# Performance work log

Measured on AMD Instinct MI355X. Metric: run time of the kernel, lower is better.

The kernel has to match this reference:

```python
import jax, jax.numpy as jnp
import numpy as np

THRESHOLD = 10.0
K = 24
EPS = 1e-9
BN_EPS = 1e-5


def setup_inputs() -> dict:
    key = jax.random.key(0)
    k0, k1, k2, k3 = jax.random.split(key, 4)
    B, C, H, W = 4, 256, 64, 64
    x = jax.random.normal(k0, (B, C, H, W), jnp.float32)
    fc_w = jax.random.normal(k1, (C, C), jnp.float32) * (1.0 / np.sqrt(C))
    fc_b = jax.random.normal(k2, (C,), jnp.float32) * 0.01
    dist_w = jax.random.normal(k3, (64, C), jnp.float32) * (1.0 / np.sqrt(C))
    bn_gamma = jnp.ones((C,), jnp.float32)
    bn_beta = jnp.zeros((C,), jnp.float32)
    return {"x": x, "fc_w": fc_w, "fc_b": fc_b, "dist_w": dist_w,
            "bn_gamma": bn_gamma, "bn_beta": bn_beta}


def reference(x, fc_w, fc_b, dist_w, bn_gamma, bn_beta):
    B, C, H, W = x.shape
    N = H * W
    # ds branch: only triggers when H == 40; here H=64 so ds=1 (no pool/interp)
    x_flat = x.reshape(B, C, N).transpose(0, 2, 1)        # [B, N, C]
    # dist_embed: 1x1 conv == linear projection per spatial location
    emb = jnp.einsum('bnc,ec->bne', x_flat, dist_w)       # [B, N, 64]
    # pairwise Euclidean distances (cdist)
    sq = jnp.sum(emb * emb, axis=-1)                      # [B, N]
    d2 = sq[:, :, None] + sq[:, None, :] - 2.0 * jnp.einsum('bne,bme->bnm', emb, emb)
    dist = jnp.sqrt(jnp.clip(d2, 0.0))                    # [B, N, N]
    # kNN mask via top_k of -dist
    _, idx = jax.lax.top_k(-dist, K)                      # [B, N, K]
    bi = jnp.arange(B)[:, None, None]
    ni = jnp.arange(N)[None, :, None]
    knn_mask = jnp.zeros((B, N, N), bool).at[bi, ni, idx].set(True)
    adj = knn_mask & (dist <= THRESHOLD)
    adj = adj | jnp.eye(N, dtype=bool)[None]
    adj_f = adj.astype(x.dtype)                           # H: [B, N, E=N]
    # HypConv: X' = Dv^{-1} H De^{-1} H^T (X Theta), residual added outside
    X_lin = x_flat @ fc_w.T + fc_b                        # [B, N, C]
    Dv = jnp.clip(jnp.sum(adj_f, axis=2), EPS, None)      # [B, N]
    De = jnp.clip(jnp.sum(adj_f, axis=1), EPS, None)      # [B, E]
    H_De_inv = adj_f / De[:, None, :]
    S = (H_De_inv @ adj_f.transpose(0, 2, 1)) / Dv[:, :, None]   # [B, N, N]
    out_flat = S @ X_lin + x_flat                         # residual
    out = out_flat.transpose(0, 2, 1).reshape(B, C, H, W)
    # BatchNorm2d in training mode (batch statistics, biased variance)
    mean = jnp.mean(out, axis=(0, 2, 3))
    var = jnp.var(out, axis=(0, 2, 3))
    o = (out - mean[None, :, None, None]) * jax.lax.rsqrt(var[None, :, None, None] + BN_EPS)
    o = o * bn_gamma[None, :, None, None] + bn_beta[None, :, None, None]
    # SiLU
    return o * jax.nn.sigmoid(o)
```

## Files before the change

### kernel.cpp

```cpp
#include <hip/hip_runtime.h>

#define NB 4096
#define BATCH 4
#define CD 256
#define ED 64
#define KNN 24

typedef __attribute__((ext_vector_type(8))) short bf16x8;
typedef __attribute__((ext_vector_type(4))) float f32x4;

__device__ __forceinline__ unsigned short f2bf(float x) {
  unsigned u = __float_as_uint(x);
  unsigned r = (u + 0x7fffu + ((u >> 16) & 1u)) >> 16;
  return (unsigned short)r;
}

__global__ __launch_bounds__(256) void k_emb(const float* __restrict__ x,
                                             const float* __restrict__ dist_w,
                                             unsigned* __restrict__ emb_hl,
                                             float* __restrict__ sq,
                                             unsigned* __restrict__ thr_g) {
  __shared__ float wds[ED * CD];
  __shared__ float red[64 * 4];
  const int b = blockIdx.x >> 6;
  const int n0 = (blockIdx.x & 63) << 6;
  const int tid = threadIdx.x;
  const float4* wsrc = (const float4*)dist_w;
  float4* wdst = (float4*)wds;
#pragma unroll
  for (int k = 0; k < 16; ++k) wdst[tid + 256 * k] = wsrc[tid + 256 * k];
  __syncthreads();
  const int eg = tid >> 6;
  const int nl = tid & 63;
  const int n = n0 + nl;
  float acc[16];
#pragma unroll
  for (int t = 0; t < 16; ++t) acc[t] = 0.f;
  const float* xb = x + (size_t)b * CD * NB + n;
#pragma unroll 2
  for (int c4 = 0; c4 < CD; c4 += 4) {
    float x0 = xb[(size_t)(c4 + 0) * NB];
    float x1 = xb[(size_t)(c4 + 1) * NB];
    float x2 = xb[(size_t)(c4 + 2) * NB];
    float x3 = xb[(size_t)(c4 + 3) * NB];
#pragma unroll
    for (int t = 0; t < 16; ++t) {
      float4 wv = *(const float4*)&wds[(eg * 16 + t) * CD + c4];
      acc[t] = fmaf(x0, wv.x, acc[t]);
      acc[t] = fmaf(x1, wv.y, acc[t]);
      acc[t] = fmaf(x2, wv.z, acc[t]);
      acc[t] = fmaf(x3, wv.w, acc[t]);
    }
  }
  float s = 0.f;
#pragma unroll
  for (int t = 0; t < 16; ++t) s = fmaf(acc[t], acc[t], s);
  unsigned hw[8], lw[8];
#pragma unroll
  for (int i = 0; i < 8; ++i) {
    unsigned short h0 = f2bf(acc[2 * i]);
    unsigned short h1 = f2bf(acc[2 * i + 1]);
    float l0f = acc[2 * i] - __uint_as_float((unsigned)h0 << 16);
    float l1f = acc[2 * i + 1] - __uint_as_float((unsigned)h1 << 16);
    hw[i] = (unsigned)h0 | ((unsigned)h1 << 16);
    lw[i] = (unsigned)f2bf(l0f) | ((unsigned)f2bf(l1f) << 16);
  }
  uint4* g = (uint4*)emb_hl;
  const size_t gb = ((size_t)(b * NB + n)) * 16;
  const int k15 = n & 15;
  g[gb + ((2 * eg) ^ k15)]     = make_uint4(hw[0], hw[1], hw[2], hw[3]);
  g[gb + ((2 * eg + 1) ^ k15)] = make_uint4(hw[4], hw[5], hw[6], hw[7]);
  g[gb + ((8 + 2 * eg) ^ k15)]     = make_uint4(lw[0], lw[1], lw[2], lw[3]);
  g[gb + ((8 + 2 * eg + 1) ^ k15)] = make_uint4(lw[4], lw[5], lw[6], lw[7]);
  red[nl * 4 + eg] = s;
  __syncthreads();
  if (tid < 64) {
    sq[b * NB + n0 + tid] = red[tid * 4] + red[tid * 4 + 1] + red[tid * 4 + 2] + red[tid * 4 + 3];
    thr_g[(b << 12) + n0 + tid] = 0x42C80000u;
  }
}

__global__ __launch_bounds__(256) void k_wsplit(const float* __restrict__ fc_w,
                                                unsigned* __restrict__ w_hl) {
  const int u = blockIdx.x * 256 + threadIdx.x;
  const int c = u >> 5, cg = u & 31;
  const int kt = cg >> 3, chl = cg & 7;
  const float* src = fc_w + (size_t)c * CD + kt * 64 + chl * 8;
  unsigned hi[4], lo[4];
#pragma unroll
  for (int j = 0; j < 4; ++j) {
    float a0 = src[2 * j], a1 = src[2 * j + 1];
    unsigned short h0 = f2bf(a0), h1 = f2bf(a1);
    float l0 = a0 - __uint_as_float((unsigned)h0 << 16);
    float l1 = a1 - __uint_as_float((unsigned)h1 << 16);
    hi[j] = (unsigned)h0 | ((unsigned)h1 << 16);
    lo[j] = (unsigned)f2bf(l0) | ((unsigned)f2bf(l1) << 16);
  }
  uint4* dst = (uint4*)w_hl;
  const int base = (c * 4 + kt) * 16;
  const int k15 = c & 15;
  dst[base + (chl ^ k15)] = make_uint4(hi[0], hi[1], hi[2], hi[3]);
  dst[base + ((chl + 8) ^ k15)] = make_uint4(lo[0], lo[1], lo[2], lo[3]);
}

__global__ __launch_bounds__(512) void k_xlin(const float* __restrict__ x,
                                              const unsigned* __restrict__ w_hl,
                                              const float* __restrict__ fc_b,
                                              float* __restrict__ xlin) {
  __shared__ __align__(16) unsigned char smem[49152];
  float* xt = (float*)smem;
  unsigned* xhl = (unsigned*)(smem + 16384);
  unsigned* whl = (unsigned*)(smem + 32768);
  const int bid = blockIdx.x;
  const int ct = bid & 3;
  const int nt = (bid >> 2) & 63;
  const int b = bid >> 8;
  const int n0 = nt << 6;
  const int tid = threadIdx.x;
  const int w = tid >> 6, lane = tid & 63;
  const int quad = lane >> 4, lr = lane & 15;
  const int rt = w >> 1;
  const int ct0 = (w & 1) * 2;
  const int rowA = rt * 16 + lr;
  const int cvt_n = tid & 63, cvt_k8 = tid >> 6;
  uint4* whl4 = (uint4*)whl;
  uint4* xhl4 = (uint4*)xhl;
  const uint4* wg = (const uint4*)w_hl;
  f32x4 acc0 = {0.f, 0.f, 0.f, 0.f};
  f32x4 acc1 = {0.f, 0.f, 0.f, 0.f};

#pragma unroll 1
  for (int kt = 0; kt < 4; ++kt) {
    __syncthreads();
#pragma unroll
    for (int i = 0; i < 8; ++i) {
      int idx = tid + 512 * i;
      int k = idx >> 6, n = idx & 63;
      xt[k * 64 + n] = x[((size_t)(b * CD + kt * 64 + k)) * NB + n0 + n];
    }
#pragma unroll
    for (int i = 0; i < 2; ++i) {
      int idx = tid + 512 * i;
      int r = idx >> 4, ch = idx & 15;
      whl4[r * 16 + ch] = wg[(size_t)((ct * 64 + r) * 4 + kt) * 16 + ch];
    }
    __syncthreads();
    {
      unsigned hi[4], lo[4];
#pragma unroll
      for (int j = 0; j < 4; ++j) {
        float a0 = xt[(cvt_k8 * 8 + 2 * j) * 64 + cvt_n];
        float a1 = xt[(cvt_k8 * 8 + 2 * j + 1) * 64 + cvt_n];
        unsigned short h0 = f2bf(a0), h1 = f2bf(a1);
        float l0 = a0 - __uint_as_float((unsigned)h0 << 16);
        float l1 = a1 - __uint_as_float((unsigned)h1 << 16);
        hi[j] = (unsigned)h0 | ((unsigned)h1 << 16);
        lo[j] = (unsigned)f2bf(l0) | ((unsigned)f2bf(l1) << 16);
      }
      const int k15 = cvt_n & 15;
      xhl4[cvt_n * 16 + (cvt_k8 ^ k15)] = make_uint4(hi[0], hi[1], hi[2], hi[3]);
      xhl4[cvt_n * 16 + ((cvt_k8 + 8) ^ k15)] = make_uint4(lo[0], lo[1], lo[2], lo[3]);
    }
    __syncthreads();
#pragma unroll
    for (int kk = 0; kk < 2; ++kk) {
      const int cb = quad + 4 * kk;
      bf16x8 a_hi = *(const bf16x8*)&xhl[rowA * 64 + ((cb) ^ lr) * 4];
      bf16x8 a_lo = *(const bf16x8*)&xhl[rowA * 64 + ((cb + 8) ^ lr) * 4];
      int rowB0 = ct0 * 16 + lr, rowB1 = rowB0 + 16;
      bf16x8 b0_hi = *(const bf16x8*)&whl[rowB0 * 64 + ((cb) ^ lr) * 4];
      bf16x8 b0_lo = *(const bf16x8*)&whl[rowB0 * 64 + ((cb + 8) ^ lr) * 4];
      bf16x8 b1_hi = *(const bf16x8*)&whl[rowB1 * 64 + ((cb) ^ lr) * 4];
      bf16x8 b1_lo = *(const bf16x8*)&whl[rowB1 * 64 + ((cb + 8) ^ lr) * 4];
      acc0 = __builtin_amdgcn_mfma_f32_16x16x32_bf16(a_hi, b0_hi, acc0, 0, 0, 0);
      acc0 = __builtin_amdgcn_mfma_f32_16x16x32_bf16(a_hi, b0_lo, acc0, 0, 0, 0);
      acc0 = __builtin_amdgcn_mfma_f32_16x16x32_bf16(a_lo, b0_hi, acc0, 0, 0, 0);
      acc1 = __builtin_amdgcn_mfma_f32_16x16x32_bf16(a_hi, b1_hi, acc1, 0, 0, 0);
      acc1 = __builtin_amdgcn_mfma_f32_16x16x32_bf16(a_hi, b1_lo, acc1, 0, 0, 0);
      acc1 = __builtin_amdgcn_mfma_f32_16x16x32_bf16(a_lo, b1_hi, acc1, 0, 0, 0);
    }
  }
#pragma unroll
  for (int reg = 0; reg < 4; ++reg) {
    int n = n0 + rt * 16 + quad * 4 + reg;
    float* dst = xlin + ((size_t)(b * NB + n)) * CD + ct * 64;
    int c0 = ct0 * 16 + lr;
    dst[c0] = acc0[reg] + fc_b[ct * 64 + c0];
    dst[c0 + 16] = acc1[reg] + fc_b[ct * 64 + c0 + 16];
  }
}

__global__ __launch_bounds__(512, 4) void k_distp(const unsigned* __restrict__ emb_hl,
                                                  const float* __restrict__ sq,
                                                  unsigned* __restrict__ thr_g,
                                                  unsigned long long* __restrict__ part) {
  __shared__ __align__(16) unsigned char smem[70400];
  unsigned* eM   = (unsigned*)smem;
  float* sqN     = (float*)(smem + 32768);
  float* sqMp    = (float*)(smem + 33024);
  unsigned* hist = (unsigned*)(smem + 35072);
  int* collectK  = (int*)(smem + 43264);
  int* cnt       = (int*)(smem + 43520);
  unsigned long long* cand = (unsigned long long*)(smem + 43776);

  const int bid = blockIdx.x;
  const int mp = bid & 7;
  const int nt = (bid >> 3) & 63;
  const int b  = bid >> 9;
  const int n0 = nt << 6;
  const int m00 = mp << 9;
  const int tid = threadIdx.x;
  const uint4* embg = (const uint4*)emb_hl;
  const size_t bbase = (size_t)b * NB;
  const int gbase = (b << 12) + n0;

  if (tid < 64) sqN[tid] = sq[b * NB + n0 + tid];
  sqMp[tid] = sq[b * NB + m00 + tid];
#pragma unroll
  for (int i = 0; i < 4; ++i) hist[tid + 512 * i] = 0;

  const int w = tid >> 6, lane = tid & 63;
  const int quad = lane >> 4, lr = lane & 15;
  const int rt = w >> 1;
  const int ct0 = (w & 1) * 2;
  const int rowA = rt * 16 + lr;
  const int rA = tid >> 4, chA = tid & 15;
  const int rB = rA + 32;

  bf16x8 aHi0 = *(const bf16x8*)&emb_hl[((bbase + n0 + rowA) * 16 + ((quad) ^ lr)) * 4];
  bf16x8 aLo0 = *(const bf16x8*)&emb_hl[((bbase + n0 + rowA) * 16 + ((quad + 8) ^ lr)) * 4];
  bf16x8 aHi1 = *(const bf16x8*)&emb_hl[((bbase + n0 + rowA) * 16 + ((quad + 4) ^ lr)) * 4];
  bf16x8 aLo1 = *(const bf16x8*)&emb_hl[((bbase + n0 + rowA) * 16 + ((quad + 12) ^ lr)) * 4];

  uint4* eM4 = (uint4*)eM;
  uint4 pf0, pf1;

#define CHUNK_MFMA_R(eMc)                                                          \
  f32x4 acc0 = {0.f, 0.f, 0.f, 0.f};                                               \
  f32x4 acc1 = {0.f, 0.f, 0.f, 0.f};                                               \
  _Pragma("unroll")                                                                \
  for (int kk = 0; kk < 2; ++kk) {                                                 \
    const int cb = quad + 4 * kk;                                                  \
    bf16x8 a_hi = kk ? aHi1 : aHi0;                                                \
    bf16x8 a_lo = kk ? aLo1 : aLo0;                                                \
    int rowB0 = ct0 * 16 + lr, rowB1 = rowB0 + 16;                                 \
    bf16x8 b0_hi = *(const bf16x8*)&(eMc)[rowB0 * 64 + ((cb) ^ lr) * 4];           \
    bf16x8 b0_lo = *(const bf16x8*)&(eMc)[rowB0 * 64 + ((cb + 8) ^ lr) * 4];       \
    bf16x8 b1_hi = *(const bf16x8*)&(eMc)[rowB1 * 64 + ((cb) ^ lr) * 4];           \
    bf16x8 b1_lo = *(const bf16x8*)&(eMc)[rowB1 * 64 + ((cb + 8) ^ lr) * 4];       \
    acc0 = __builtin_amdgcn_mfma_f32_16x16x32_bf16(a_hi, b0_hi, acc0, 0, 0, 0);    \
    acc0 = __builtin_amdgcn_mfma_f32_16x16x32_bf16(a_hi, b0_lo, acc0, 0, 0, 0);    \
    acc0 = __builtin_amdgcn_mfma_f32_16x16x32_bf16(a_lo, b0_hi, acc0, 0, 0, 0);    \
    acc1 = __builtin_amdgcn_mfma_f32_16x16x32_bf16(a_hi, b1_hi, acc1, 0, 0, 0);    \
    acc1 = __builtin_amdgcn_mfma_f32_16x16x32_bf16(a_hi, b1_lo, acc1, 0, 0, 0);    \
    acc1 = __builtin_amdgcn_mfma_f32_16x16x32_bf16(a_lo, b1_hi, acc1, 0, 0, 0);    \
  }

#define STAGE_PROLOGUE()                                             \
  pf0 = embg[(bbase + m00 + rA) * 16 + chA];                         \
  pf1 = embg[(bbase + m00 + rB) * 16 + chA];                         \
  eM4[rA * 16 + chA] = pf0;                                          \
  eM4[rB * 16 + chA] = pf1;                                          \
  pf0 = embg[(bbase + m00 + 64 + rA) * 16 + chA];                    \
  pf1 = embg[(bbase + m00 + 64 + rB) * 16 + chA];

#define RESTAGE_DB(ci_)                                              \
  if ((ci_) < 7) {                                                   \
    uint4* dst = eM4 + (((ci_) + 1) & 1) * 1024;                     \
    dst[rA * 16 + chA] = pf0;                                        \
    dst[rB * 16 + chA] = pf1;                                        \
    if ((ci_) < 6) {                                                 \
      pf0 = embg[(bbase + m00 + ((ci_) + 2) * 64 + rA) * 16 + chA];  \
      pf1 = embg[(bbase + m00 + ((ci_) + 2) * 64 + rB) * 16 + chA];  \
    }                                                                \
  }

  STAGE_PROLOGUE()
#pragma unroll 1
  for (int ci = 0; ci < 8; ++ci) {
    const int m0 = ci << 6;
    __syncthreads();
    const unsigned* eMc = eM + (ci & 1) * 4096;
    CHUNK_MFMA_R(eMc)
#pragma unroll
    for (int reg = 0; reg < 4; ++reg) {
      int row = rt * 16 + quad * 4 + reg;
      int c0 = ct0 * 16 + lr, c1 = c0 + 16;
      float d20 = fmaxf(sqN[row] + sqMp[m0 + c0] - 2.f * acc0[reg], 0.f);
      float d21 = fmaxf(sqN[row] + sqMp[m0 + c1] - 2.f * acc1[reg], 0.f);
      if (__float_as_uint(d20) <= 0x42C80000u) {
        int bk0 = min(63, (int)(d20 * 0.64f));
        atomicAdd(&hist[bk0 * 32 + (row >> 1)], 1u << (16 * (row & 1)));
      }
      if (__float_as_uint(d21) <= 0x42C80000u) {
        int bk1 = min(63, (int)(d21 * 0.64f));
        atomicAdd(&hist[bk1 * 32 + (row >> 1)], 1u << (16 * (row & 1)));
      }
    }
    RESTAGE_DB(ci)
  }
  __syncthreads();

  if (tid < 64) {
    int cum = 0, kb = 63;
    const int sh = 16 * (tid & 1);
#pragma unroll 1
    for (int k2 = 0; k2 < 64; ++k2) {
      cum += (hist[k2 * 32 + (tid >> 1)] >> sh) & 0xFFFFu;
      if (cum >= 24) { kb = k2; break; }
    }
    float edge = (float)(kb + 2) * 1.5625f;
    atomicMin(&thr_g[gbase + tid], __float_as_uint(edge));
    unsigned tg = thr_g[gbase + tid];
    int kImp = min(63, (int)(__uint_as_float(tg) * 0.64f));
    collectK[tid] = min(kb, kImp);
    cnt[tid] = 0;
  }
#pragma unroll
  for (int i = 0; i < 7; ++i) {
    int q = tid + 512 * i;
    if (q < 64 * 52) cand[q] = ~0ULL;
  }
  __syncthreads();

  STAGE_PROLOGUE()
#pragma unroll 1
  for (int ci = 0; ci < 8; ++ci) {
    const int m0 = ci << 6;
    __syncthreads();
    const unsigned* eMc = eM + (ci & 1) * 4096;
    CHUNK_MFMA_R(eMc)
#pragma unroll
    for (int reg = 0; reg < 4; ++reg) {
      int row = rt * 16 + quad * 4 + reg;
      int c0 = ct0 * 16 + lr, c1 = c0 + 16;
      float d20 = fmaxf(sqN[row] + sqMp[m0 + c0] - 2.f * acc0[reg], 0.f);
      float d21 = fmaxf(sqN[row] + sqMp[m0 + c1] - 2.f * acc1[reg], 0.f);
      int kc = collectK[row];
      unsigned bi0 = __float_as_uint(d20), bi1 = __float_as_uint(d21);
      int bk0 = min(63, (int)(d20 * 0.64f));
      int bk1 = min(63, (int)(d21 * 0.64f));
      if (bk0 <= kc && bi0 <= 0x42C80000u) {
        int pos = atomicAdd(&cnt[row], 1);
        if (pos < 52) cand[row * 52 + pos] = ((unsigned long long)bi0 << 32) | (unsigned)(m00 + m0 + c0);
      }
      if (bk1 <= kc && bi1 <= 0x42C80000u) {
        int pos = atomicAdd(&cnt[row], 1);
        if (pos < 52) cand[row * 52 + pos] = ((unsigned long long)bi1 << 32) | (unsigned)(m00 + m0 + c1);
      }
    }
    RESTAGE_DB(ci)
  }
  __syncthreads();

  {
    const int row8 = tid >> 3, sub = tid & 7;
    unsigned long long last = 0;
    unsigned long long* op = part + ((size_t)bid * 64 + row8) * 24;
#pragma unroll 1
    for (int k = 0; k < 24; ++k) {
      unsigned long long lm = ~0ULL;
#pragma unroll
      for (int j2 = 0; j2 < 7; ++j2) {
        int p2 = sub + 8 * j2;
        if (p2 < 52) {
          unsigned long long v2 = cand[row8 * 52 + p2];
          if ((k == 0 || v2 > last) && v2 < lm) lm = v2;
        }
      }
#pragma unroll
      for (int s2 = 1; s2 < 8; s2 <<= 1) {
        unsigned long long o2 = __shfl_xor(lm, s2);
        if (o2 < lm) lm = o2;
      }
      if (sub == 0) op[k] = lm;
      last = lm;
    }
  }
}

__global__ __launch_bounds__(64) void k_merge(const unsigned long long* __restrict__ part,
                                              int* __restrict__ row_idx,
                                              int* __restrict__ row_cnt,
                                              int* __restrict__ col_cnt) {
  const int row = blockIdx.x * 64 + threadIdx.x;
  const int b = row >> 12;
  const int n = row & 4095;
  const int nt = n >> 6, r = n & 63;
  const size_t gb = (size_t)(((b << 6) | nt) << 3);
  unsigned long long h[8];
  int pp[8];
#pragma unroll
  for (int t = 0; t < 8; ++t) {
    h[t] = part[((gb + t) * 64 + r) * 24];
    pp[t] = 0;
  }
  int cnt = 0;
  const int base = row * KNN;
  for (int k = 0; k < 24; ++k) {
    int bs = 0;
    unsigned long long mv = h[0];
#pragma unroll
    for (int t = 1; t < 8; ++t)
      if (h[t] < mv) { mv = h[t]; bs = t; }
    if ((unsigned)(mv >> 32) > 0x42C80000u) break;
    int mi = (int)(mv & 0xFFFFFFFFu);
    row_idx[base + cnt] = mi;
    atomicAdd(&col_cnt[(b << 12) + mi], 1);
    ++cnt;
    int np = ++pp[bs];
    h[bs] = (np < 24) ? part[((gb + bs) * 64 + r) * 24 + np] : ~0ULL;
  }
  row_cnt[row] = cnt;
#pragma unroll 4
  for (int j = cnt; j < 24; ++j) row_idx[base + j] = n;
}

__global__ __launch_bounds__(256) void k_scan(const int* __restrict__ col_cnt,
                                              int* __restrict__ col_start,
                                              int* __restrict__ col_cursor) {
  __shared__ int part[256];
  const int tid = threadIdx.x;
  const int base = tid * 64;
  int s = 0;
  for (int j = 0; j < 64; ++j) s += col_cnt[base + j];
  part[tid] = s;
  __syncthreads();
  for (int off = 1; off < 256; off <<= 1) {
    int v = (tid >= off) ? part[tid - off] : 0;
    __syncthreads();
    part[tid] += v;
    __syncthreads();
  }
  int run = part[tid] - s;
  for (int j = 0; j < 64; ++j) {
    col_start[base + j] = run;
    col_cursor[base + j] = run;
    run += col_cnt[base + j];
  }
}

__global__ __launch_bounds__(64) void k_fill(const int* __restrict__ row_idx,
                                             const int* __restrict__ row_cnt,
                                             int* __restrict__ col_cursor,
                                             int* __restrict__ col_list) {
  const int row = blockIdx.x * 64 + threadIdx.x;
  const int b = row >> 12;
  const int cnt = row_cnt[row];
  for (int j = 0; j < cnt; ++j) {
    int m = row_idx[row * KNN + j];
    int pos = atomicAdd(&col_cursor[(b << 12) + m], 1);
    col_list[pos] = row & 4095;
  }
}

__global__ __launch_bounds__(256) void k_yd(const float* __restrict__ xlin,
                                            const int* __restrict__ col_cnt,
                                            const int* __restrict__ col_start,
                                            const int* __restrict__ col_list,
                                            float* __restrict__ yd) {
  const int le = threadIdx.x >> 6;
  const int c4 = threadIdx.x & 63;
  const int be = blockIdx.x * 4 + le;
  const int b = be >> 12;
  const int deg = col_cnt[be];
  const int start = col_start[be];
  float4 acc = make_float4(0.f, 0.f, 0.f, 0.f);
  int j = 0;
  for (; j + 3 < deg; j += 4) {
    int ma = col_list[start + j], mb2 = col_list[start + j + 1];
    int mc = col_list[start + j + 2], md = col_list[start + j + 3];
    float4 va = *(const float4*)&xlin[(((size_t)(b << 12) + ma) << 8) + c4 * 4];
    float4 vb = *(const float4*)&xlin[(((size_t)(b << 12) + mb2) << 8) + c4 * 4];
    float4 vc = *(const float4*)&xlin[(((size_t)(b << 12) + mc) << 8) + c4 * 4];
    float4 vd = *(const float4*)&xlin[(((size_t)(b << 12) + md) << 8) + c4 * 4];
    acc.x += (va.x + vb.x) + (vc.x + vd.x);
    acc.y += (va.y + vb.y) + (vc.y + vd.y);
    acc.z += (va.z + vb.z) + (vc.z + vd.z);
    acc.w += (va.w + vb.w) + (vc.w + vd.w);
  }
  for (; j < deg; ++j) {
    int m = col_list[start + j];
    float4 v = *(const float4*)&xlin[(((size_t)(b << 12) + m) << 8) + c4 * 4];
    acc.x += v.x; acc.y += v.y; acc.z += v.z; acc.w += v.w;
  }
  float inv = 1.f / (float)deg;
  acc.x *= inv; acc.y *= inv; acc.z *= inv; acc.w *= inv;
  *(float4*)&yd[((size_t)be << 8) + c4 * 4] = acc;
}

__global__ __launch_bounds__(256) void k_out2(const float* __restrict__ yd,
                                              const int* __restrict__ row_idx,
                                              const int* __restrict__ row_cnt,
                                              float* __restrict__ outf) {
  const int b = blockIdx.x >> 8;
  const int nt = blockIdx.x & 255;
  const int le = threadIdx.x >> 6;
  const int c4 = threadIdx.x & 63;
  for (int ii = 0; ii < 4; ++ii) {
    int n = nt * 16 + le * 4 + ii;
    int row = (b << 12) + n;
    int cnt = row_cnt[row];
    int idx[24];
    const int4* ip = (const int4*)(row_idx + (size_t)row * KNN);
#pragma unroll
    for (int t = 0; t < 6; ++t) {
      int4 v = ip[t];
      idx[4 * t] = v.x; idx[4 * t + 1] = v.y; idx[4 * t + 2] = v.z; idx[4 * t + 3] = v.w;
    }
    float4 acc = make_float4(0.f, 0.f, 0.f, 0.f);
#pragma unroll
    for (int j = 0; j < 24; ++j) {
      float wgt = (j < cnt) ? 1.f : 0.f;
      float4 v = *(const float4*)&yd[(((size_t)(b << 12) + idx[j]) << 8) + c4 * 4];
      acc.x = fmaf(wgt, v.x, acc.x);
      acc.y = fmaf(wgt, v.y, acc.y);
      acc.z = fmaf(wgt, v.z, acc.z);
      acc.w = fmaf(wgt, v.w, acc.w);
    }
    float inv = 1.f / (float)cnt;
    acc.x *= inv; acc.y *= inv; acc.z *= inv; acc.w *= inv;
    *(float4*)&outf[((size_t)row << 8) + c4 * 4] = acc;
  }
}

__global__ __launch_bounds__(256) void k_res_bn(const float* __restrict__ x,
                                                float* __restrict__ outf,
                                                float* __restrict__ bn_sum,
                                                float* __restrict__ bn_sumsq) {
  __shared__ float xt[256 * 69];
  const int b = blockIdx.x >> 6;
  const int n0 = (blockIdx.x & 63) << 6;
  const int tid = threadIdx.x;
#pragma unroll 4
  for (int k = 0; k < 16; ++k) {
    int q = tid + 256 * k;
    int c = q >> 4, f = q & 15;
    float4 v = *(const float4*)&x[((size_t)(b * CD + c)) * NB + n0 + 4 * f];
    xt[c * 69 + 4 * f + 0] = v.x;
    xt[c * 69 + 4 * f + 1] = v.y;
    xt[c * 69 + 4 * f + 2] = v.z;
    xt[c * 69 + 4 * f + 3] = v.w;
  }
  __syncthreads();
  float s = 0.f, q = 0.f;
  const size_t rbase = ((size_t)((b << 12) + n0)) << 8;
#pragma unroll 4
  for (int i = 0; i < 64; ++i) {
    float v = outf[rbase + (size_t)i * 256 + tid] + xt[tid * 69 + i];
    outf[rbase + (size_t)i * 256 + tid] = v;
    s += v;
    q = fmaf(v, v, q);
  }
  atomicAdd(&bn_sum[tid], s);
  atomicAdd(&bn_sumsq[tid], q);
}

__global__ __launch_bounds__(256) void k_write(const float* __restrict__ outf,
                                               const float* __restrict__ bn_sum,
                                               const float* __restrict__ bn_sumsq,
                                               const float* __restrict__ gamma,
                                               const float* __restrict__ beta,
                                               float* __restrict__ out) {
  __shared__ float tile[64 * 257];
  __shared__ float sc[256], sh[256];
  const int b = blockIdx.x >> 6;
  const int n0 = (blockIdx.x & 63) << 6;
  const int tid = threadIdx.x;
  {
    const float inv = 1.f / 16384.f;
    float mean = bn_sum[tid] * inv;
    float var = bn_sumsq[tid] * inv - mean * mean;
    float scf = gamma[tid] * rsqrtf(var + 1e-5f);
    sc[tid] = scf;
    sh[tid] = beta[tid] - mean * scf;
  }
  __syncthreads();
#pragma unroll 4
  for (int i = 0; i < 64; ++i) {
    int idx = tid + 256 * i;
    int n = idx >> 8, c = idx & 255;
    float v = outf[(((size_t)(b << 12) + n0 + n) << 8) + c];
    v = fmaf(v, sc[c], sh[c]);
    float w = v / (1.f + expf(-v));
    tile[n * 257 + c] = w;
  }
  __syncthreads();
  const int nl = tid & 63;
  const int cg = tid >> 6;
#pragma unroll 4
  for (int j = 0; j < 64; ++j) {
    int c = cg * 64 + j;
    out[((size_t)(b * CD + c)) * NB + n0 + nl] = tile[nl * 257 + c];
  }
}

extern "C" void kernel_launch(void* const* d_in, const int* in_sizes, int n_in,
                              void* d_out, int out_size, void* d_ws, size_t ws_size,
                              hipStream_t stream) {
  const float* x      = (const float*)d_in[0];
  const float* fc_w   = (const float*)d_in[1];
  const float* fc_b   = (const float*)d_in[2];
  const float* dist_w = (const float*)d_in[3];
  const float* gamma  = (const float*)d_in[4];
  const float* beta   = (const float*)d_in[5];
  float* out = (float*)d_out;
  char* ws = (char*)d_ws;

  const size_t OFF_EHL   = 0;
  const size_t OFF_XLIN  = (size_t)4 << 20;
  const size_t OFF_YD    = (size_t)20 << 20;
  const size_t OFF_OUTF  = (size_t)36 << 20;
  const size_t OFF_SQ    = (size_t)52 << 20;
  const size_t OFF_RIDX  = OFF_SQ + 65536;
  const size_t OFF_RCNT  = OFF_RIDX + 1572864;
  const size_t OFF_CCNT  = OFF_RCNT + 65536;
  const size_t OFF_CSTART = OFF_CCNT + 65536;
  const size_t OFF_CCUR  = OFF_CSTART + 65536;
  const size_t OFF_CLIST = OFF_CCUR + 65536;
  const size_t OFF_BNS   = OFF_CLIST + 1572864;
  const size_t OFF_BNQ   = OFF_BNS + 1024;
  const size_t OFF_THRG  = OFF_BNQ + 1024;
  const size_t OFF_WHL   = OFF_THRG + 65536;
  const size_t TOTAL = OFF_WHL + 262144;
  if (ws_size < TOTAL) return;

  unsigned* emb_hl = (unsigned*)(ws + OFF_EHL);
  float* xlin  = (float*)(ws + OFF_XLIN);
  float* yd    = (float*)(ws + OFF_YD);
  float* outf  = (float*)(ws + OFF_OUTF);
  unsigned long long* part = (unsigned long long*)(ws + OFF_YD);
  float* sq    = (float*)(ws + OFF_SQ);
  int* row_idx = (int*)(ws + OFF_RIDX);
  int* row_cnt = (int*)(ws + OFF_RCNT);
  int* col_cnt = (int*)(ws + OFF_CCNT);
  int* col_start = (int*)(ws + OFF_CSTART);
  int* col_cursor = (int*)(ws + OFF_CCUR);
  int* col_list = (int*)(ws + OFF_CLIST);
  float* bn_sum = (float*)(ws + OFF_BNS);
  float* bn_sumsq = (float*)(ws + OFF_BNQ);
  unsigned* thr_g = (unsigned*)(ws + OFF_THRG);
  unsigned* w_hl = (unsigned*)(ws + OFF_WHL);

  hipMemsetAsync(col_cnt, 0, 65536, stream);
  hipMemsetAsync(bn_sum, 0, 2048, stream);

  k_emb<<<256, 256, 0, stream>>>(x, dist_w, emb_hl, sq, thr_g);
  k_wsplit<<<32, 256, 0, stream>>>(fc_w, w_hl);
  k_xlin<<<1024, 512, 0, stream>>>(x, w_hl, fc_b, xlin);
  k_distp<<<2048, 512, 0, stream>>>(emb_hl, sq, thr_g, part);
  k_merge<<<256, 64, 0, stream>>>(part, row_idx, row_cnt, col_cnt);
  k_scan<<<1, 256, 0, stream>>>(col_cnt, col_start, col_cursor);
  k_fill<<<256, 64, 0, stream>>>(row_idx, row_cnt, col_cursor, col_list);
  k_yd<<<4096, 256, 0, stream>>>(xlin, col_cnt, col_start, col_list, yd);
  k_out2<<<1024, 256, 0, stream>>>(yd, row_idx, row_cnt, outf);
  k_res_bn<<<256, 256, 0, stream>>>(x, outf, bn_sum, bn_sumsq);
  k_write<<<256, 256, 0, stream>>>(outf, bn_sum, bn_sumsq, gamma, beta, out);
}
```

Baseline: 491.1 us.

## Store X_lin as bf16 and shrink k_distp LDS for higher occupancy

X_lin is now written in bf16, which halves the bytes gathered in k_yd, and k_yd widens values back to fp32 when accumulating. k_distp drops double-buffered LDS staging in favour of a single buffer with an extra barrier per chunk, and shrinks the per-row candidate list from 52 to 48 entries. Together these cut shared memory enough to raise the occupancy hint from 4 to 6 blocks. The costs are bf16 rounding error in the aggregation, lost copy/compute overlap in the distance loop, and a small risk of overflowing the smaller candidate buffer.

```diff
diff --git a/kernel.cpp b/kernel.cpp
--- a/kernel.cpp
+++ b/kernel.cpp
@@ -106,7 +106,7 @@
 __global__ __launch_bounds__(512) void k_xlin(const float* __restrict__ x,
                                               const unsigned* __restrict__ w_hl,
                                               const float* __restrict__ fc_b,
-                                              float* __restrict__ xlin) {
+                                              unsigned short* __restrict__ xlin_h) {
   __shared__ __align__(16) unsigned char smem[49152];
   float* xt = (float*)smem;
   unsigned* xhl = (unsigned*)(smem + 16384);
@@ -183,25 +183,25 @@
 #pragma unroll
   for (int reg = 0; reg < 4; ++reg) {
     int n = n0 + rt * 16 + quad * 4 + reg;
-    float* dst = xlin + ((size_t)(b * NB + n)) * CD + ct * 64;
+    unsigned short* dst = xlin_h + (((size_t)(b * NB + n)) << 8) + ct * 64;
     int c0 = ct0 * 16 + lr;
-    dst[c0] = acc0[reg] + fc_b[ct * 64 + c0];
-    dst[c0 + 16] = acc1[reg] + fc_b[ct * 64 + c0 + 16];
-  }
-}
-
-__global__ __launch_bounds__(512, 4) void k_distp(const unsigned* __restrict__ emb_hl,
+    dst[c0] = f2bf(acc0[reg] + fc_b[ct * 64 + c0]);
+    dst[c0 + 16] = f2bf(acc1[reg] + fc_b[ct * 64 + c0 + 16]);
+  }
+}
+
+__global__ __launch_bounds__(512, 6) void k_distp(const unsigned* __restrict__ emb_hl,
                                                   const float* __restrict__ sq,
                                                   unsigned* __restrict__ thr_g,
                                                   unsigned long long* __restrict__ part) {
-  __shared__ __align__(16) unsigned char smem[70400];
+  __shared__ __align__(16) unsigned char smem[51968];
   unsigned* eM   = (unsigned*)smem;
-  float* sqN     = (float*)(smem + 32768);
-  float* sqMp    = (float*)(smem + 33024);
-  unsigned* hist = (unsigned*)(smem + 35072);
-  int* collectK  = (int*)(smem + 43264);
-  int* cnt       = (int*)(smem + 43520);
-  unsigned long long* cand = (unsigned long long*)(smem + 43776);
+  float* sqN     = (float*)(smem + 16384);
+  float* sqMp    = (float*)(smem + 16640);
+  unsigned* hist = (unsigned*)(smem + 18688);
+  int* collectK  = (int*)(smem + 26880);
+  int* cnt       = (int*)(smem + 27136);
+  unsigned long long* cand = (unsigned long long*)(smem + 27392);
 
   const int bid = blockIdx.x;
   const int mp = bid & 7;
@@ -235,7 +235,7 @@
   uint4* eM4 = (uint4*)eM;
   uint4 pf0, pf1;
 
-#define CHUNK_MFMA_R(eMc)                                                          \
+#define CHUNK_MFMA_R()                                                             \
   f32x4 acc0 = {0.f, 0.f, 0.f, 0.f};                                               \
   f32x4 acc1 = {0.f, 0.f, 0.f, 0.f};                                               \
   _Pragma("unroll")                                                                \
@@ -244,10 +244,10 @@
     bf16x8 a_hi = kk ? aHi1 : aHi0;                                                \
     bf16x8 a_lo = kk ? aLo1 : aLo0;                                                \
     int rowB0 = ct0 * 16 + lr, rowB1 = rowB0 + 16;                                 \
-    bf16x8 b0_hi = *(const bf16x8*)&(eMc)[rowB0 * 64 + ((cb) ^ lr) * 4];           \
-    bf16x8 b0_lo = *(const bf16x8*)&(eMc)[rowB0 * 64 + ((cb + 8) ^ lr) * 4];       \
-    bf16x8 b1_hi = *(const bf16x8*)&(eMc)[rowB1 * 64 + ((cb) ^ lr) * 4];           \
-    bf16x8 b1_lo = *(const bf16x8*)&(eMc)[rowB1 * 64 + ((cb + 8) ^ lr) * 4];       \
+    bf16x8 b0_hi = *(const bf16x8*)&eM[rowB0 * 64 + ((cb) ^ lr) * 4];              \
+    bf16x8 b0_lo = *(const bf16x8*)&eM[rowB0 * 64 + ((cb + 8) ^ lr) * 4];          \
+    bf16x8 b1_hi = *(const bf16x8*)&eM[rowB1 * 64 + ((cb) ^ lr) * 4];              \
+    bf16x8 b1_lo = *(const bf16x8*)&eM[rowB1 * 64 + ((cb + 8) ^ lr) * 4];          \
     acc0 = __builtin_amdgcn_mfma_f32_16x16x32_bf16(a_hi, b0_hi, acc0, 0, 0, 0);    \
     acc0 = __builtin_amdgcn_mfma_f32_16x16x32_bf16(a_hi, b0_lo, acc0, 0, 0, 0);    \
     acc0 = __builtin_amdgcn_mfma_f32_16x16x32_bf16(a_lo, b0_hi, acc0, 0, 0, 0);    \
@@ -256,7 +256,7 @@
     acc1 = __builtin_amdgcn_mfma_f32_16x16x32_bf16(a_lo, b1_hi, acc1, 0, 0, 0);    \
   }
 
-#define STAGE_PROLOGUE()                                             \
+#define STAGE_FIRST()                                                \
   pf0 = embg[(bbase + m00 + rA) * 16 + chA];                         \
   pf1 = embg[(bbase + m00 + rB) * 16 + chA];                         \
   eM4[rA * 16 + chA] = pf0;                                          \
@@ -264,24 +264,22 @@
   pf0 = embg[(bbase + m00 + 64 + rA) * 16 + chA];                    \
   pf1 = embg[(bbase + m00 + 64 + rB) * 16 + chA];
 
-#define RESTAGE_DB(ci_)                                              \
+#define RESTAGE(ci_)                                                 \
   if ((ci_) < 7) {                                                   \
-    uint4* dst = eM4 + (((ci_) + 1) & 1) * 1024;                     \
-    dst[rA * 16 + chA] = pf0;                                        \
-    dst[rB * 16 + chA] = pf1;                                        \
+    eM4[rA * 16 + chA] = pf0;                                        \
+    eM4[rB * 16 + chA] = pf1;                                        \
     if ((ci_) < 6) {                                                 \
       pf0 = embg[(bbase + m00 + ((ci_) + 2) * 64 + rA) * 16 + chA];  \
       pf1 = embg[(bbase + m00 + ((ci_) + 2) * 64 + rB) * 16 + chA];  \
     }                                                                \
   }
 
-  STAGE_PROLOGUE()
+  STAGE_FIRST()
 #pragma unroll 1
   for (int ci = 0; ci < 8; ++ci) {
     const int m0 = ci << 6;
     __syncthreads();
-    const unsigned* eMc = eM + (ci & 1) * 4096;
-    CHUNK_MFMA_R(eMc)
+    CHUNK_MFMA_R()
 #pragma unroll
     for (int reg = 0; reg < 4; ++reg) {
       int row = rt * 16 + quad * 4 + reg;
@@ -297,7 +295,8 @@
         atomicAdd(&hist[bk1 * 32 + (row >> 1)], 1u << (16 * (row & 1)));
       }
     }
-    RESTAGE_DB(ci)
+    __syncthreads();
+    RESTAGE(ci)
   }
   __syncthreads();
 
@@ -317,19 +316,17 @@
     cnt[tid] = 0;
   }
 #pragma unroll
-  for (int i = 0; i < 7; ++i) {
-    int q = tid + 512 * i;
-    if (q < 64 * 52) cand[q] = ~0ULL;
-  }
-  __syncthreads();
-
-  STAGE_PROLOGUE()
+  for (int i = 0; i < 6; ++i) {
+    cand[tid + 512 * i] = ~0ULL;
+  }
+  __syncthreads();
+
+  STAGE_FIRST()
 #pragma unroll 1
   for (int ci = 0; ci < 8; ++ci) {
     const int m0 = ci << 6;
     __syncthreads();
-    const unsigned* eMc = eM + (ci & 1) * 4096;
-    CHUNK_MFMA_R(eMc)
+    CHUNK_MFMA_R()
 #pragma unroll
     for (int reg = 0; reg < 4; ++reg) {
       int row = rt * 16 + quad * 4 + reg;
@@ -342,14 +339,15 @@
       int bk1 = min(63, (int)(d21 * 0.64f));
       if (bk0 <= kc && bi0 <= 0x42C80000u) {
         int pos = atomicAdd(&cnt[row], 1);
-        if (pos < 52) cand[row * 52 + pos] = ((unsigned long long)bi0 << 32) | (unsigned)(m00 + m0 + c0);
+        if (pos < 48) cand[row * 48 + pos] = ((unsigned long long)bi0 << 32) | (unsigned)(m00 + m0 + c0);
       }
       if (bk1 <= kc && bi1 <= 0x42C80000u) {
         int pos = atomicAdd(&cnt[row], 1);
-        if (pos < 52) cand[row * 52 + pos] = ((unsigned long long)bi1 << 32) | (unsigned)(m00 + m0 + c1);
+        if (pos < 48) cand[row * 48 + pos] = ((unsigned long long)bi1 << 32) | (unsigned)(m00 + m0 + c1);
       }
     }
-    RESTAGE_DB(ci)
+    __syncthreads();
+    RESTAGE(ci)
   }
   __syncthreads();
 
@@ -361,12 +359,10 @@
     for (int k = 0; k < 24; ++k) {
       unsigned long long lm = ~0ULL;
 #pragma unroll
-      for (int j2 = 0; j2 < 7; ++j2) {
+      for (int j2 = 0; j2 < 6; ++j2) {
         int p2 = sub + 8 * j2;
-        if (p2 < 52) {
-          unsigned long long v2 = cand[row8 * 52 + p2];
-          if ((k == 0 || v2 > last) && v2 < lm) lm = v2;
-        }
+        unsigned long long v2 = cand[row8 * 48 + p2];
+        if ((k == 0 || v2 > last) && v2 < lm) lm = v2;
       }
 #pragma unroll
       for (int s2 = 1; s2 < 8; s2 <<= 1) {
@@ -454,7 +450,7 @@
   }
 }
 
-__global__ __launch_bounds__(256) void k_yd(const float* __restrict__ xlin,
+__global__ __launch_bounds__(256) void k_yd(const unsigned short* __restrict__ xlin_h,
                                             const int* __restrict__ col_cnt,
                                             const int* __restrict__ col_start,
                                             const int* __restrict__ col_list,
@@ -466,23 +462,26 @@
   const int deg = col_cnt[be];
   const int start = col_start[be];
   float4 acc = make_float4(0.f, 0.f, 0.f, 0.f);
+#define BF2F_LO(u) __uint_as_float(((u) & 0xFFFFu) << 16)
+#define BF2F_HI(u) __uint_as_float((u) & 0xFFFF0000u)
   int j = 0;
   for (; j + 3 < deg; j += 4) {
     int ma = col_list[start + j], mb2 = col_list[start + j + 1];
     int mc = col_list[start + j + 2], md = col_list[start + j + 3];
-    float4 va = *(const float4*)&xlin[(((size_t)(b << 12) + ma) << 8) + c4 * 4];
-    float4 vb = *(const float4*)&xlin[(((size_t)(b << 12) + mb2) << 8) + c4 * 4];
-    float4 vc = *(const float4*)&xlin[(((size_t)(b << 12) + mc) << 8) + c4 * 4];
-    float4 vd = *(const float4*)&xlin[(((size_t)(b << 12) + md) << 8) + c4 * 4];
-    acc.x += (va.x + vb.x) + (vc.x + vd.x);
-    acc.y += (va.y + vb.y) + (vc.y + vd.y);
-    acc.z += (va.z + vb.z) + (vc.z + vd.z);
-    acc.w += (va.w + vb.w) + (vc.w + vd.w);
+    uint2 va = *(const uint2*)&xlin_h[(((size_t)(b << 12) + ma) << 8) + c4 * 4];
+    uint2 vb = *(const uint2*)&xlin_h[(((size_t)(b << 12) + mb2) << 8) + c4 * 4];
+    uint2 vc = *(const uint2*)&xlin_h[(((size_t)(b << 12) + mc) << 8) + c4 * 4];
+    uint2 vd = *(const uint2*)&xlin_h[(((size_t)(b << 12) + md) << 8) + c4 * 4];
+    acc.x += (BF2F_LO(va.x) + BF2F_LO(vb.x)) + (BF2F_LO(vc.x) + BF2F_LO(vd.x));
+    acc.y += (BF2F_HI(va.x) + BF2F_HI(vb.x)) + (BF2F_HI(vc.x) + BF2F_HI(vd.x));
+    acc.z += (BF2F_LO(va.y) + BF2F_LO(vb.y)) + (BF2F_LO(vc.y) + BF2F_LO(vd.y));
+    acc.w += (BF2F_HI(va.y) + BF2F_HI(vb.y)) + (BF2F_HI(vc.y) + BF2F_HI(vd.y));
   }
   for (; j < deg; ++j) {
     int m = col_list[start + j];
-    float4 v = *(const float4*)&xlin[(((size_t)(b << 12) + m) << 8) + c4 * 4];
-    acc.x += v.x; acc.y += v.y; acc.z += v.z; acc.w += v.w;
+    uint2 v = *(const uint2*)&xlin_h[(((size_t)(b << 12) + m) << 8) + c4 * 4];
+    acc.x += BF2F_LO(v.x); acc.y += BF2F_HI(v.x);
+    acc.z += BF2F_LO(v.y); acc.w += BF2F_HI(v.y);
   }
   float inv = 1.f / (float)deg;
   acc.x *= inv; acc.y *= inv; acc.z *= inv; acc.w *= inv;
@@ -626,7 +625,7 @@
   if (ws_size < TOTAL) return;
 
   unsigned* emb_hl = (unsigned*)(ws + OFF_EHL);
-  float* xlin  = (float*)(ws + OFF_XLIN);
+  unsigned short* xlin_h = (unsigned short*)(ws + OFF_XLIN);
   float* yd    = (float*)(ws + OFF_YD);
   float* outf  = (float*)(ws + OFF_OUTF);
   unsigned long long* part = (unsigned long long*)(ws + OFF_YD);
@@ -647,12 +646,12 @@
 
   k_emb<<<256, 256, 0, stream>>>(x, dist_w, emb_hl, sq, thr_g);
   k_wsplit<<<32, 256, 0, stream>>>(fc_w, w_hl);
-  k_xlin<<<1024, 512, 0, stream>>>(x, w_hl, fc_b, xlin);
+  k_xlin<<<1024, 512, 0, stream>>>(x, w_hl, fc_b, xlin_h);
   k_distp<<<2048, 512, 0, stream>>>(emb_hl, sq, thr_g, part);
   k_merge<<<256, 64, 0, stream>>>(part, row_idx, row_cnt, col_cnt);
   k_scan<<<1, 256, 0, stream>>>(col_cnt, col_start, col_cursor);
   k_fill<<<256, 64, 0, stream>>>(row_idx, row_cnt, col_cursor, col_list);
-  k_yd<<<4096, 256, 0, stream>>>(xlin, col_cnt, col_start, col_list, yd);
+  k_yd<<<4096, 256, 0, stream>>>(xlin_h, col_cnt, col_start, col_list, yd);
   k_out2<<<1024, 256, 0, stream>>>(yd, row_idx, row_cnt, outf);
   k_res_bn<<<256, 256, 0, stream>>>(x, outf, bn_sum, bn_sumsq);
   k_write<<<256, 256, 0, stream>>>(outf, bn_sum, bn_sumsq, gamma, beta, out);
```

Result: faster. 450.4 us (-8.3%).
